# Optimization experiments

Measured on AMD Instinct MI355X. Metric: run time of the kernel, lower is better.

Reference implementation:

```python
import jax, jax.numpy as jnp
import numpy as np

CH, XH, YH, RADIUS = 2, 2, 2, 1  # channel_heads, x_heads, y_heads, neighborhood radius


def neighborhood_mask(n_sub_x, n_sub_y, radius):
    # clamped neighbor offsets reduce to |di|<=r and |dj|<=r within the grid
    iy = jnp.arange(n_sub_y)
    ix = jnp.arange(n_sub_x)
    my = jnp.abs(iy[:, None] - iy[None, :]) <= radius  # [ny, ny]
    mx = jnp.abs(ix[:, None] - ix[None, :]) <= radius  # [nx, nx]
    m = my[:, None, :, None] & mx[None, :, None, :]    # [ny, nx, ny, nx]
    s = n_sub_x * n_sub_y
    return m.reshape(s, s)  # row-major (h1 w1)(h2 w2), matching einops


def setup_inputs() -> dict:
    key = jax.random.key(0)
    k1, k2, k3 = jax.random.split(key, 3)
    C = 128
    seq = jax.random.normal(k1, (2, 256, C, 16, 16), dtype=jnp.float32)
    w_qkv = jax.random.normal(k2, (3 * C, C), dtype=jnp.float32) / np.sqrt(C).astype(np.float32)
    w_out = jax.random.normal(k3, (C, C), dtype=jnp.float32) / np.sqrt(C).astype(np.float32)
    b_out = jnp.zeros((C,), dtype=jnp.float32)
    return {"seq": seq, "w_qkv": w_qkv, "w_out": w_out, "b_out": b_out,
            "n_sub_x": 16, "n_sub_y": 16}


def reference(seq, w_qkv, w_out, b_out, n_sub_x, n_sub_y):
    b, s, C, H, W = seq.shape
    h, w = H // YH, W // XH
    c = C // CH
    nH = YH * XH * CH  # total heads

    # pointwise qkv projection over channels: [b, s, 3C, H, W]
    qkv = jnp.einsum('bschw,dc->bsdhw', seq, w_qkv)

    # decompose2d: split spatial grid into y_heads x x_heads blocks -> spatial heads
    # [b, s, 3C, YH, h, XH, w] -> [b, s, YH*XH, 3C, h, w]
    qkv = qkv.reshape(b, s, 3 * C, YH, h, XH, w)
    qkv = qkv.transpose(0, 1, 3, 5, 2, 4, 6).reshape(b, s, YH * XH, 3 * C, h, w)

    # split into q,k,v and channel heads: 3C = 3 * CH * c
    qkv = qkv.reshape(b, s, YH * XH, 3, CH, c, h, w)
    # -> [3, b, (spatial_heads * channel_heads), s, c, h, w]
    qkv = qkv.transpose(3, 0, 2, 4, 1, 5, 6, 7).reshape(3, b, nH, s, c, h, w)
    q, k, v = qkv[0], qkv[1], qkv[2]

    # scaled dot-product attention over flattened function dim (c,h,w)
    scale = 1.0 / np.sqrt(c * h * w).astype(np.float32)
    scores = jnp.einsum('bnschw,bntchw->bnst', q, k) * scale  # [b, nH, s, s]
    mask = neighborhood_mask(n_sub_x, n_sub_y, RADIUS)  # [s, s]
    scores = jnp.where(mask[None, None, :, :], scores, jnp.finfo(scores.dtype).min)
    attn = jax.nn.softmax(scores, axis=-1)
    sa = jnp.einsum('bnst,bntchw->bnschw', attn, v)  # [b, nH, s, c, h, w]

    # merge channel heads back: [b, s, spatial_heads, C, h, w]
    sa = sa.reshape(b, YH * XH, CH, s, c, h, w)
    sa = sa.transpose(0, 3, 1, 2, 4, 5, 6).reshape(b, s, YH, XH, C, h, w)
    # recompose2d: [b, s, C, H, W]
    sa = sa.transpose(0, 1, 4, 2, 5, 3, 6).reshape(b, s, C, H, W)

    # output pointwise projection with bias
    out = jnp.einsum('bschw,dc->bsdhw', sa, w_out) + b_out[None, None, :, None, None]
    return out
```

## Files before the change

### kernel.cpp

```cpp
#include <hip/hip_runtime.h>

#define BATCH 2
#define SS    256
#define CC    128
#define HWN   256
#define FDIM  4096

typedef unsigned int uint;
typedef unsigned short ushort;
typedef short bf16x8 __attribute__((ext_vector_type(8)));
typedef ushort us4 __attribute__((ext_vector_type(4)));
typedef float f32x4 __attribute__((ext_vector_type(4)));

__device__ __forceinline__ ushort f2b(float f) {
  uint u = __float_as_uint(f);
  return (ushort)((u + 0x7fffu + ((u >> 16) & 1u)) >> 16);
}
__device__ __forceinline__ float b2f(ushort h) { return __uint_as_float((uint)h << 16); }

__global__ void k_convert(const float* __restrict__ wqkv, const float* __restrict__ wout,
                          ushort* __restrict__ wqkv_b, ushort* __restrict__ wout_b) {
  int i = blockIdx.x * 256 + threadIdx.x;
  if (i < 384 * 128) wqkv_b[i] = f2b(wqkv[i]);
  if (i < 128 * 128) {
    const int cc = i & 127;
    const int ks = cc >> 5, qq = (cc >> 3) & 3, j = cc & 7;
    const int creal = (ks >> 1) * 64 + ((((ks & 1) << 1) | (qq >> 1)) << 4)
                      + ((qq & 1) << 3) + j;
    wout_b[i] = f2b(wout[(i >> 7) * 128 + creal]);
  }
}

__global__ __launch_bounds__(256) void k_qkv(const float* __restrict__ seq,
                                             const ushort* __restrict__ wqkv_b,
                                             ushort* __restrict__ qkvh) {
  __shared__ ushort wlds[128 * 128];
  const int blk = blockIdx.x;
  const int bs = blk >> 2, hq = blk & 3;
  const int b = bs >> 8, s = bs & 255;
  const int t = threadIdx.x;
  const int wave = t >> 6, lane = t & 63;
  const int qq = lane >> 4, m = lane & 15;
  const int ntg = hq * 4 + wave;
  const int hw = ntg * 16 + m;

  const float* sp = seq + (size_t)bs * (CC * HWN);

  bf16x8 bfrag[4];
  #pragma unroll
  for (int ks = 0; ks < 4; ++ks) {
    const int k0 = ks * 32 + qq * 8;
    float tmp[8];
    #pragma unroll
    for (int j = 0; j < 8; ++j) tmp[j] = sp[(k0 + j) * HWN + hw];
    bf16x8 fr;
    #pragma unroll
    for (int j = 0; j < 8; ++j) fr[j] = (short)f2b(tmp[j]);
    bfrag[ks] = fr;
  }

  const int n_qk = ((ntg >> 3) * 2 + (m >> 3)) * 2;
  const int hwl  = (ntg & 7) * 8 + (m & 7);

  for (int qkvi = 0; qkvi < 3; ++qkvi) {
    if (qkvi > 0) __syncthreads();
    #pragma unroll
    for (int i = 0; i < 8; ++i) {
      const int row = i * 16 + (t >> 4), col16 = t & 15;
      bf16x8 w = *(const bf16x8*)(wqkv_b + (qkvi * 128 + row) * 128 + col16 * 8);
      *(bf16x8*)&wlds[row * 128 + ((col16 ^ (row & 15)) * 8)] = w;
    }
    __syncthreads();

    #pragma unroll
    for (int mt8 = 0; mt8 < 8; ++mt8) {
      bf16x8 afrag[4];
      #pragma unroll
      for (int ks = 0; ks < 4; ++ks)
        afrag[ks] = *(const bf16x8*)&wlds[(mt8 * 16 + m) * 128 + (((ks * 4 + qq) ^ m) * 8)];
      const int ch = mt8 >> 2, m4 = mt8 & 3;
      f32x4 acc = {0.f, 0.f, 0.f, 0.f};
      #pragma unroll
      for (int ks = 0; ks < 4; ++ks)
        acc = __builtin_amdgcn_mfma_f32_16x16x32_bf16(afrag[ks], bfrag[ks], acc, 0, 0, 0);
      const int n = n_qk + ch;
      const size_t base = ((size_t)(qkvi * 16 + b * 8 + n) * SS + s) * FDIM;
      us4 pk;
      #pragma unroll
      for (int r = 0; r < 4; ++r) pk[r] = f2b(acc[r]);
      *(us4*)(qkvh + base + m4 * 1024 + hwl * 16 + qq * 4) = pk;
    }
  }
}

__global__ __launch_bounds__(1024) void k_scores(const ushort* __restrict__ qkvh,
                                                 float* __restrict__ attn) {
  __shared__ float red[16][64][12];
  const int g = blockIdx.x;
  const int unit = (g & 7) * 32 + (g >> 3);
  const int b  = unit >> 7;
  const int n  = (unit >> 4) & 7;
  const int sy = unit & 15;
  const int t = threadIdx.x;
  const int wave = t >> 6, lane = t & 63;
  const int qq = lane >> 4, l15 = lane & 15;
  const size_t hs = (size_t)SS * FDIM;
  const ushort* qb = qkvh + (size_t)(b * 8 + n) * hs;
  const ushort* kb = qkvh + (size_t)(16 + b * 8 + n) * hs;

  const ushort* qp = qb + (size_t)(sy * 16 + l15) * FDIM + qq * 8;
  const ushort* kp[3];
  #pragma unroll
  for (int tl = 0; tl < 3; ++tl) {
    const int tyc = min(max(sy - 1 + tl, 0), 15);
    kp[tl] = kb + (size_t)(tyc * 16 + l15) * FDIM + qq * 8;
  }

  f32x4 acc[3] = {{0,0,0,0},{0,0,0,0},{0,0,0,0}};
  const int kbeg = wave * 256;
  #pragma unroll
  for (int it = 0; it < 4; ++it) {
    const int k0 = kbeg + it * 64;
    bf16x8 a0 = *(const bf16x8*)(qp + k0);
    bf16x8 a1 = *(const bf16x8*)(qp + k0 + 32);
    bf16x8 b0[3], b1[3];
    #pragma unroll
    for (int tl = 0; tl < 3; ++tl) {
      b0[tl] = *(const bf16x8*)(kp[tl] + k0);
      b1[tl] = *(const bf16x8*)(kp[tl] + k0 + 32);
    }
    #pragma unroll
    for (int tl = 0; tl < 3; ++tl)
      acc[tl] = __builtin_amdgcn_mfma_f32_16x16x32_bf16(a0, b0[tl], acc[tl], 0, 0, 0);
    #pragma unroll
    for (int tl = 0; tl < 3; ++tl)
      acc[tl] = __builtin_amdgcn_mfma_f32_16x16x32_bf16(a1, b1[tl], acc[tl], 0, 0, 0);
  }

  #pragma unroll
  for (int tl = 0; tl < 3; ++tl)
    #pragma unroll
    for (int r = 0; r < 4; ++r) red[wave][lane][tl * 4 + r] = acc[tl][r];
  __syncthreads();
  if (t < 768) {
    const int lane2 = t / 12, idx = t - lane2 * 12;
    float ssum = red[0][lane2][idx];
    #pragma unroll
    for (int w = 1; w < 16; ++w) ssum += red[w][lane2][idx];
    red[0][lane2][idx] = ssum;
  }
  __syncthreads();
  if (wave != 0) return;
  #pragma unroll
  for (int tl = 0; tl < 3; ++tl)
    #pragma unroll
    for (int r = 0; r < 4; ++r) acc[tl][r] = red[0][lane][tl * 4 + r];

  const int tx = l15;
  float sc[3][4];
  #pragma unroll
  for (int tl = 0; tl < 3; ++tl) {
    const int ty = sy - 1 + tl;
    const bool tyv = (ty >= 0 && ty < 16);
    #pragma unroll
    for (int r = 0; r < 4; ++r) {
      const int sx = qq * 4 + r;
      const bool v = tyv && (tx - sx <= 1) && (sx - tx <= 1);
      sc[tl][r] = v ? acc[tl][r] * (1.f / 64.f) : -1e30f;
    }
  }
  #pragma unroll
  for (int r = 0; r < 4; ++r) {
    float mx = fmaxf(fmaxf(sc[0][r], sc[1][r]), sc[2][r]);
    #pragma unroll
    for (int off = 1; off < 16; off <<= 1) mx = fmaxf(mx, __shfl_xor(mx, off));
    float p[3], sum = 0.f;
    #pragma unroll
    for (int tl = 0; tl < 3; ++tl) { p[tl] = __expf(sc[tl][r] - mx); sum += p[tl]; }
    #pragma unroll
    for (int off = 1; off < 16; off <<= 1) sum += __shfl_xor(sum, off);
    const float inv = 1.f / sum;
    const int sx = qq * 4 + r;
    const int s = sy * 16 + sx;
    #pragma unroll
    for (int tl = 0; tl < 3; ++tl) {
      const int ty = sy - 1 + tl;
      const int dxp = tx - sx + 1;
      if (ty >= 0 && ty < 16 && dxp >= 0 && dxp <= 2)
        attn[((size_t)(b * 8 + n) * SS + s) * 9 + tl * 3 + dxp] = p[tl] * inv;
    }
  }
}

__global__ __launch_bounds__(256) void k_out(const ushort* __restrict__ qkvh,
                                             const float* __restrict__ attn,
                                             const ushort* __restrict__ wout_b,
                                             const float* __restrict__ bout,
                                             float* __restrict__ out) {
  __shared__ ushort wlds[128 * 128];
  const int g = blockIdx.x;
  const int r9 = g >> 3;
  const int G = (g & 7) * 4 + (r9 >> 6);
  const int idx = r9 & 63;
  const int b = G >> 4, sy = G & 15;
  const int sx = idx >> 2, sub = idx & 3;
  const int s = sy * 16 + sx;
  const int bs = b * 256 + s;
  const int t = threadIdx.x;
  const int wave = t >> 6, lane = t & 63;
  const int ntg = sub * 4 + wave;
  const int qq = lane >> 4, m = lane & 15;
  const size_t hs = (size_t)SS * FDIM;

  #pragma unroll
  for (int i = 0; i < 8; ++i) {
    const int row = i * 16 + (t >> 4), col16 = t & 15;
    bf16x8 w = *(const bf16x8*)(wout_b + row * 128 + col16 * 8);
    *(bf16x8*)&wlds[row * 128 + ((col16 ^ (row & 15)) * 8)] = w;
  }

  int sjc[9];
  bool vld[9];
  #pragma unroll
  for (int j = 0; j < 9; ++j) {
    const int ny = sy + j / 3 - 1, nx = sx + j % 3 - 1;
    vld[j] = (ny >= 0 && ny < 16 && nx >= 0 && nx < 16);
    sjc[j] = min(max(ny, 0), 15) * 16 + min(max(nx, 0), 15);
  }

  const int nbase = ((ntg >> 3) * 2 + (m >> 3)) * 2;
  float pch[2][9];
  #pragma unroll
  for (int ch = 0; ch < 2; ++ch) {
    #pragma unroll
    for (int j = 0; j < 9; ++j) {
      const float w = attn[((size_t)(b * 8 + nbase + ch) * SS + s) * 9 + j];
      pch[ch][j] = vld[j] ? w : 0.f;
    }
  }

  const int hwl = (ntg & 7) * 8 + (m & 7);
  bf16x8 bfrag[4];
  #pragma unroll
  for (int ks = 0; ks < 4; ++ks) {
    const int ch = ks >> 1;
    const int c64hi = ((ks & 1) << 1) | (qq >> 1);
    const int half = qq & 1;
    const ushort* vb = qkvh + (size_t)(32 + b * 8 + nbase + ch) * hs;
    const int off = c64hi * 1024 + hwl * 16 + half * 8;
    float facc[8] = {0.f, 0.f, 0.f, 0.f, 0.f, 0.f, 0.f, 0.f};
    #pragma unroll
    for (int j = 0; j < 9; ++j) {
      bf16x8 vv = *(const bf16x8*)(vb + (size_t)sjc[j] * FDIM + off);
      const float pj = pch[ch][j];
      #pragma unroll
      for (int e = 0; e < 8; ++e) facc[e] += pj * b2f((ushort)vv[e]);
    }
    bf16x8 fr;
    #pragma unroll
    for (int e = 0; e < 8; ++e) fr[e] = (short)f2b(facc[e]);
    bfrag[ks] = fr;
  }

  __syncthreads();

  #pragma unroll
  for (int mt = 0; mt < 8; ++mt) {
    bf16x8 afrag[4];
    #pragma unroll
    for (int ks = 0; ks < 4; ++ks)
      afrag[ks] = *(const bf16x8*)&wlds[(mt * 16 + m) * 128 + (((ks * 4 + qq) ^ m) * 8)];
    f32x4 acc = {0.f, 0.f, 0.f, 0.f};
    #pragma unroll
    for (int ks = 0; ks < 4; ++ks)
      acc = __builtin_amdgcn_mfma_f32_16x16x32_bf16(afrag[ks], bfrag[ks], acc, 0, 0, 0);
    const int hw = ntg * 16 + m;
    #pragma unroll
    for (int r = 0; r < 4; ++r) {
      const int d = mt * 16 + qq * 4 + r;
      out[((size_t)bs * CC + d) * HWN + hw] = acc[r] + bout[d];
    }
  }
}

extern "C" void kernel_launch(void* const* d_in, const int* in_sizes, int n_in,
                              void* d_out, int out_size, void* d_ws, size_t ws_size,
                              hipStream_t stream) {
  const float* seq  = (const float*)d_in[0];
  const float* wqkv = (const float*)d_in[1];
  const float* wout = (const float*)d_in[2];
  const float* bout = (const float*)d_in[3];
  char* ws = (char*)d_ws;
  ushort* wqkv_b = (ushort*)(ws);
  ushort* wout_b = (ushort*)(ws + 98304);
  ushort* qkvh   = (ushort*)(ws + 131072);
  float*  attn   = (float*)(ws + 131072 + 100663296ull);
  float*  outp   = (float*)d_out;

  hipLaunchKernelGGL(k_convert, dim3(192),  dim3(256), 0, stream, wqkv, wout, wqkv_b, wout_b);
  hipLaunchKernelGGL(k_qkv,     dim3(2048), dim3(256), 0, stream, seq, wqkv_b, qkvh);
  hipLaunchKernelGGL(k_scores,  dim3(256),  dim3(1024), 0, stream, qkvh, attn);
  hipLaunchKernelGGL(k_out,     dim3(2048), dim3(256), 0, stream, qkvh, attn, wout_b, bout, outp);
}
```

Baseline: 190.0 us.

## Process four column tiles per wave to amortize weight staging in qkv and out kernels

Each block now handles a whole (b,s) slab instead of a quarter, with each wave holding four sets of B fragments and reusing every LDS weight A-fragment across four MFMA groups. This cuts the number of blocks that reload the 32KB weight tile into LDS by four, in both the qkv projection and the output projection. The cost is more registers per thread (launch bounds of 2 blocks per CU), a grid of 512 blocks instead of 2048, and a changed block-to-(b,s) mapping in k_out that may alter cache locality for the neighbor V reads.

Result: no change. 192.3 us (+1.2%).

```diff
diff --git a/kernel.cpp b/kernel.cpp
--- a/kernel.cpp
+++ b/kernel.cpp
@@ -31,39 +31,42 @@
   }
 }
 
-__global__ __launch_bounds__(256) void k_qkv(const float* __restrict__ seq,
-                                             const ushort* __restrict__ wqkv_b,
-                                             ushort* __restrict__ qkvh) {
+__global__ __launch_bounds__(256, 2) void k_qkv(const float* __restrict__ seq,
+                                                const ushort* __restrict__ wqkv_b,
+                                                ushort* __restrict__ qkvh) {
   __shared__ ushort wlds[128 * 128];
-  const int blk = blockIdx.x;
-  const int bs = blk >> 2, hq = blk & 3;
+  const int bs = blockIdx.x;
   const int b = bs >> 8, s = bs & 255;
   const int t = threadIdx.x;
-  const int wave = t >> 6, lane = t & 63;
+  const int hq = t >> 6, lane = t & 63;
   const int qq = lane >> 4, m = lane & 15;
-  const int ntg = hq * 4 + wave;
-  const int hw = ntg * 16 + m;
 
   const float* sp = seq + (size_t)bs * (CC * HWN);
 
-  bf16x8 bfrag[4];
-  #pragma unroll
-  for (int ks = 0; ks < 4; ++ks) {
-    const int k0 = ks * 32 + qq * 8;
-    float tmp[8];
-    #pragma unroll
-    for (int j = 0; j < 8; ++j) tmp[j] = sp[(k0 + j) * HWN + hw];
-    bf16x8 fr;
-    #pragma unroll
-    for (int j = 0; j < 8; ++j) fr[j] = (short)f2b(tmp[j]);
-    bfrag[ks] = fr;
-  }
-
-  const int n_qk = ((ntg >> 3) * 2 + (m >> 3)) * 2;
-  const int hwl  = (ntg & 7) * 8 + (m & 7);
+  bf16x8 bfrag[4][4];
+  uint obase[4];
+  #pragma unroll
+  for (int set = 0; set < 4; ++set) {
+    const int ntg = hq * 4 + set;
+    const int hw = ntg * 16 + m;
+    #pragma unroll
+    for (int ks = 0; ks < 4; ++ks) {
+      const int k0 = ks * 32 + qq * 8;
+      float tmp[8];
+      #pragma unroll
+      for (int j = 0; j < 8; ++j) tmp[j] = sp[(k0 + j) * HWN + hw];
+      bf16x8 fr;
+      #pragma unroll
+      for (int j = 0; j < 8; ++j) fr[j] = (short)f2b(tmp[j]);
+      bfrag[set][ks] = fr;
+    }
+    const int n_qk = ((ntg >> 3) * 2 + (m >> 3)) * 2;
+    const int hwl  = (ntg & 7) * 8 + (m & 7);
+    obase[set] = (uint)(((b * 8 + n_qk) * SS + s) * FDIM + hwl * 16 + qq * 4);
+  }
 
   for (int qkvi = 0; qkvi < 3; ++qkvi) {
-    if (qkvi > 0) __syncthreads();
+    if (qkvi) __syncthreads();
     #pragma unroll
     for (int i = 0; i < 8; ++i) {
       const int row = i * 16 + (t >> 4), col16 = t & 15;
@@ -79,16 +82,18 @@
       for (int ks = 0; ks < 4; ++ks)
         afrag[ks] = *(const bf16x8*)&wlds[(mt8 * 16 + m) * 128 + (((ks * 4 + qq) ^ m) * 8)];
       const int ch = mt8 >> 2, m4 = mt8 & 3;
-      f32x4 acc = {0.f, 0.f, 0.f, 0.f};
-      #pragma unroll
-      for (int ks = 0; ks < 4; ++ks)
-        acc = __builtin_amdgcn_mfma_f32_16x16x32_bf16(afrag[ks], bfrag[ks], acc, 0, 0, 0);
-      const int n = n_qk + ch;
-      const size_t base = ((size_t)(qkvi * 16 + b * 8 + n) * SS + s) * FDIM;
-      us4 pk;
-      #pragma unroll
-      for (int r = 0; r < 4; ++r) pk[r] = f2b(acc[r]);
-      *(us4*)(qkvh + base + m4 * 1024 + hwl * 16 + qq * 4) = pk;
+      #pragma unroll
+      for (int set = 0; set < 4; ++set) {
+        f32x4 acc = {0.f, 0.f, 0.f, 0.f};
+        #pragma unroll
+        for (int ks = 0; ks < 4; ++ks)
+          acc = __builtin_amdgcn_mfma_f32_16x16x32_bf16(afrag[ks], bfrag[set][ks], acc, 0, 0, 0);
+        us4 pk;
+        #pragma unroll
+        for (int r = 0; r < 4; ++r) pk[r] = f2b(acc[r]);
+        *(us4*)(qkvh + obase[set]
+                + (uint)((qkvi * 16 + ch) * (SS * FDIM) + m4 * 1024)) = pk;
+      }
     }
   }
 }
@@ -192,23 +197,18 @@
   }
 }
 
-__global__ __launch_bounds__(256) void k_out(const ushort* __restrict__ qkvh,
-                                             const float* __restrict__ attn,
-                                             const ushort* __restrict__ wout_b,
-                                             const float* __restrict__ bout,
-                                             float* __restrict__ out) {
+__global__ __launch_bounds__(256, 2) void k_out(const ushort* __restrict__ qkvh,
+                                                const float* __restrict__ attn,
+                                                const ushort* __restrict__ wout_b,
+                                                const float* __restrict__ bout,
+                                                float* __restrict__ out) {
   __shared__ ushort wlds[128 * 128];
   const int g = blockIdx.x;
-  const int r9 = g >> 3;
-  const int G = (g & 7) * 4 + (r9 >> 6);
-  const int idx = r9 & 63;
-  const int b = G >> 4, sy = G & 15;
-  const int sx = idx >> 2, sub = idx & 3;
-  const int s = sy * 16 + sx;
-  const int bs = b * 256 + s;
+  const int bs = (g & 7) * 64 + (g >> 3);
+  const int b = bs >> 8, s = bs & 255;
+  const int sy = s >> 4, sx = s & 15;
   const int t = threadIdx.x;
-  const int wave = t >> 6, lane = t & 63;
-  const int ntg = sub * 4 + wave;
+  const int sub = t >> 6, lane = t & 63;
   const int qq = lane >> 4, m = lane & 15;
   const size_t hs = (size_t)SS * FDIM;
 
@@ -228,38 +228,43 @@
     sjc[j] = min(max(ny, 0), 15) * 16 + min(max(nx, 0), 15);
   }
 
-  const int nbase = ((ntg >> 3) * 2 + (m >> 3)) * 2;
-  float pch[2][9];
-  #pragma unroll
-  for (int ch = 0; ch < 2; ++ch) {
-    #pragma unroll
-    for (int j = 0; j < 9; ++j) {
-      const float w = attn[((size_t)(b * 8 + nbase + ch) * SS + s) * 9 + j];
-      pch[ch][j] = vld[j] ? w : 0.f;
-    }
-  }
-
-  const int hwl = (ntg & 7) * 8 + (m & 7);
-  bf16x8 bfrag[4];
-  #pragma unroll
-  for (int ks = 0; ks < 4; ++ks) {
-    const int ch = ks >> 1;
-    const int c64hi = ((ks & 1) << 1) | (qq >> 1);
-    const int half = qq & 1;
-    const ushort* vb = qkvh + (size_t)(32 + b * 8 + nbase + ch) * hs;
-    const int off = c64hi * 1024 + hwl * 16 + half * 8;
-    float facc[8] = {0.f, 0.f, 0.f, 0.f, 0.f, 0.f, 0.f, 0.f};
-    #pragma unroll
-    for (int j = 0; j < 9; ++j) {
-      bf16x8 vv = *(const bf16x8*)(vb + (size_t)sjc[j] * FDIM + off);
-      const float pj = pch[ch][j];
-      #pragma unroll
-      for (int e = 0; e < 8; ++e) facc[e] += pj * b2f((ushort)vv[e]);
-    }
-    bf16x8 fr;
-    #pragma unroll
-    for (int e = 0; e < 8; ++e) fr[e] = (short)f2b(facc[e]);
-    bfrag[ks] = fr;
+  bf16x8 bfrag[4][4];
+  #pragma unroll
+  for (int set = 0; set < 4; ++set) {
+    const int ntg = sub * 4 + set;
+    const int nbase = ((ntg >> 3) * 2 + (m >> 3)) * 2;
+    const int hwl = (ntg & 7) * 8 + (m & 7);
+
+    float pch[2][9];
+    #pragma unroll
+    for (int ch = 0; ch < 2; ++ch) {
+      #pragma unroll
+      for (int j = 0; j < 9; ++j) {
+        const float w = attn[((size_t)(b * 8 + nbase + ch) * SS + s) * 9 + j];
+        pch[ch][j] = vld[j] ? w : 0.f;
+      }
+    }
+
+    #pragma unroll
+    for (int ks = 0; ks < 4; ++ks) {
+      const int ch = ks >> 1;
+      const int c64hi = ((ks & 1) << 1) | (qq >> 1);
+      const int half = qq & 1;
+      const ushort* vb = qkvh + (size_t)(32 + b * 8 + nbase + ch) * hs;
+      const int off = c64hi * 1024 + hwl * 16 + half * 8;
+      float facc[8] = {0.f, 0.f, 0.f, 0.f, 0.f, 0.f, 0.f, 0.f};
+      #pragma unroll
+      for (int j = 0; j < 9; ++j) {
+        bf16x8 vv = *(const bf16x8*)(vb + (size_t)sjc[j] * FDIM + off);
+        const float pj = pch[ch][j];
+        #pragma unroll
+        for (int e = 0; e < 8; ++e) facc[e] += pj * b2f((ushort)vv[e]);
+      }
+      bf16x8 fr;
+      #pragma unroll
+      for (int e = 0; e < 8; ++e) fr[e] = (short)f2b(facc[e]);
+      bfrag[set][ks] = fr;
+    }
   }
 
   __syncthreads();
@@ -270,15 +275,18 @@
     #pragma unroll
     for (int ks = 0; ks < 4; ++ks)
       afrag[ks] = *(const bf16x8*)&wlds[(mt * 16 + m) * 128 + (((ks * 4 + qq) ^ m) * 8)];
-    f32x4 acc = {0.f, 0.f, 0.f, 0.f};
-    #pragma unroll
-    for (int ks = 0; ks < 4; ++ks)
-      acc = __builtin_amdgcn_mfma_f32_16x16x32_bf16(afrag[ks], bfrag[ks], acc, 0, 0, 0);
-    const int hw = ntg * 16 + m;
-    #pragma unroll
-    for (int r = 0; r < 4; ++r) {
-      const int d = mt * 16 + qq * 4 + r;
-      out[((size_t)bs * CC + d) * HWN + hw] = acc[r] + bout[d];
+    #pragma unroll
+    for (int set = 0; set < 4; ++set) {
+      f32x4 acc = {0.f, 0.f, 0.f, 0.f};
+      #pragma unroll
+      for (int ks = 0; ks < 4; ++ks)
+        acc = __builtin_amdgcn_mfma_f32_16x16x32_bf16(afrag[ks], bfrag[set][ks], acc, 0, 0, 0);
+      const int hw = (sub * 4 + set) * 16 + m;
+      #pragma unroll
+      for (int r = 0; r < 4; ++r) {
+        const int d = mt * 16 + qq * 4 + r;
+        out[((size_t)bs * CC + d) * HWN + hw] = acc[r] + bout[d];
+      }
     }
   }
 }
@@ -297,8 +305,8 @@
   float*  attn   = (float*)(ws + 131072 + 100663296ull);
   float*  outp   = (float*)d_out;
 
-  hipLaunchKernelGGL(k_convert, dim3(192),  dim3(256), 0, stream, wqkv, wout, wqkv_b, wout_b);
-  hipLaunchKernelGGL(k_qkv,     dim3(2048), dim3(256), 0, stream, seq, wqkv_b, qkvh);
-  hipLaunchKernelGGL(k_scores,  dim3(256),  dim3(1024), 0, stream, qkvh, attn);
-  hipLaunchKernelGGL(k_out,     dim3(2048), dim3(256), 0, stream, qkvh, attn, wout_b, bout, outp);
-}
+  hipLaunchKernelGGL(k_convert, dim3(192), dim3(256), 0, stream, wqkv, wout, wqkv_b, wout_b);
+  hipLaunchKernelGGL(k_qkv,     dim3(512), dim3(256), 0, stream, seq, wqkv_b, qkvh);
+  hipLaunchKernelGGL(k_scores,  dim3(256), dim3(1024), 0, stream, qkvh, attn);
+  hipLaunchKernelGGL(k_out,     dim3(512), dim3(256), 0, stream, qkvh, attn, wout_b, bout, outp);
+}
```
